# Performance work log

Measured on AMD Instinct MI355X. Metric: run time of the kernel, lower is better.

## Reference

```python
import jax, jax.numpy as jnp
import numpy as np
import math

DIM = 256
B, T = 4, 4096

def setup_inputs() -> dict:
    key = jax.random.key(0)
    ks = jax.random.split(key, 16)
    d = DIM
    def lin(k, dout, din):
        bound = 1.0 / math.sqrt(din)
        kw, kb = jax.random.split(k)
        W = jax.random.uniform(kw, (dout, din), minval=-bound, maxval=bound, dtype=jnp.float32)
        b = jax.random.uniform(kb, (dout,), minval=-bound, maxval=bound, dtype=jnp.float32)
        return W, b
    x = jax.random.normal(ks[0], (B, T, d), dtype=jnp.float32)
    wq, bq = lin(ks[1], d, d)
    wk, bk = lin(ks[2], d, d)
    wv, bv = lin(ks[3], d, d)
    wo, bo = lin(ks[4], d, d)
    w1, b1 = lin(ks[5], 4 * d, d)
    w2, b2 = lin(ks[6], d, 4 * d)
    return {
        "x": x,
        "attn_norm_w": jnp.ones((d,), jnp.float32),
        "mlp_norm_w": jnp.ones((d,), jnp.float32),
        "wq": wq, "bq": bq, "wk": wk, "bk": bk, "wv": wv, "bv": bv,
        "wo": wo, "bo": bo, "w1": w1, "b1": b1, "w2": w2, "b2": b2,
    }

def _rms_norm(x, w, eps=1e-6):
    rms = jnp.sqrt(jnp.mean(x * x, axis=-1, keepdims=True) + eps)
    return x / rms * w

def reference(x, attn_norm_w, mlp_norm_w, wq, bq, wk, bk, wv, bv, wo, bo, w1, b1, w2, b2):
    b, t, d = x.shape
    xn = _rms_norm(x, attn_norm_w)
    q = xn @ wq.T + bq  # [b,t,d]
    k = xn @ wk.T + bk
    v = xn @ wv.T + bv
    scores = jnp.einsum('btd,bsd->bts', q, k) / math.sqrt(d)
    causal = jnp.tril(jnp.ones((t, t), dtype=bool))
    scores = jnp.where(causal, scores, -1e9)
    probs = jax.nn.softmax(scores, axis=-1)
    attn = jnp.einsum('bts,bsd->btd', probs, v)
    x = x + attn @ wo.T + bo
    hn = _rms_norm(x, mlp_norm_w)
    h = jax.nn.gelu(hn @ w1.T + b1, approximate=False)
    return x + h @ w2.T + b2
```

## Files before the change

### kernel.cpp

```cpp
#include <hip/hip_runtime.h>

typedef __attribute__((ext_vector_type(8))) short bfrag;
typedef __attribute__((ext_vector_type(4))) float f32x4;

__device__ __forceinline__ f32x4 mfma16(bfrag a, bfrag b, f32x4 c) {
    return __builtin_amdgcn_mfma_f32_16x16x32_bf16(a, b, c, 0, 0, 0);
}
__device__ __forceinline__ unsigned short f2bf(float f) {
    unsigned int u = __float_as_uint(f);
    u = u + 0x7fffu + ((u >> 16) & 1u);
    return (unsigned short)(u >> 16);
}
__device__ __forceinline__ void glds16(const unsigned short* g, unsigned short* l) {
    __builtin_amdgcn_global_load_lds(
        (const __attribute__((address_space(1))) void*)g,
        (__attribute__((address_space(3))) void*)l, 16, 0, 0);
}

#define DIM 256
#define BT  16384
#define TSEQ 4096
#define FB   1048576


__global__ __launch_bounds__(256) void k_prep(
    const float* __restrict__ x, const float* __restrict__ anw,
    const float* __restrict__ wq, const float* __restrict__ wk,
    const float* __restrict__ wv, const float* __restrict__ wo,
    const float* __restrict__ w1, const float* __restrict__ w2,
    unsigned short* __restrict__ wqF, unsigned short* __restrict__ wkF,
    unsigned short* __restrict__ wvF, unsigned short* __restrict__ woF,
    unsigned short* __restrict__ w1F, unsigned short* __restrict__ w2F,
    unsigned short* __restrict__ xnF)
{
    int bid = blockIdx.x;
    int wave = threadIdx.x >> 6, lane = threadIdx.x & 63;
    int q = lane >> 4, r = lane & 15;
    if (bid < 384) {
        int fid = bid * 4 + wave;
        const float* src; unsigned short* dst; int ntile, ks, K, fbase;
        if (fid < 512) {
            int w = fid >> 7, fl = fid & 127;
            ntile = fl >> 3; ks = fl & 7; K = 256;
            src = (w == 0) ? wq : (w == 1) ? wk : (w == 2) ? wv : wo;
            dst = (w == 0) ? wqF : (w == 1) ? wkF : (w == 2) ? wvF : woF;
            fbase = (ntile * 8 + ks) * 512;
        } else if (fid < 1024) {
            int fl = fid - 512;
            ntile = fl >> 3; ks = fl & 7; K = 256;
            src = w1; dst = w1F;
            fbase = (ntile * 8 + ks) * 512;
        } else {
            int fl = fid - 1024;
            ntile = fl >> 5; ks = fl & 31; K = 1024;
            src = w2; dst = w2F;
            fbase = (ntile * 32 + ks) * 512;
        }
        const float* s = src + (ntile * 16 + r) * K + ks * 32 + q * 8;
        float4 v0 = *(const float4*)(s);
        float4 v1 = *(const float4*)(s + 4);
        unsigned short o[8] = { f2bf(v0.x), f2bf(v0.y), f2bf(v0.z), f2bf(v0.w),
                                f2bf(v1.x), f2bf(v1.y), f2bf(v1.z), f2bf(v1.w) };
        *(ushort4*)(dst + fbase + lane * 8)     = make_ushort4(o[0], o[1], o[2], o[3]);
        *(ushort4*)(dst + fbase + lane * 8 + 4) = make_ushort4(o[4], o[5], o[6], o[7]);
    } else {
        int row  = (bid - 384) * 4 + wave;
        float4 v = *(const float4*)(x + row * DIM + lane * 4);
        float ss = v.x*v.x + v.y*v.y + v.z*v.z + v.w*v.w;
        #pragma unroll
        for (int off = 1; off < 64; off <<= 1) ss += __shfl_xor(ss, off);
        float inv = rsqrtf(ss * (1.0f / DIM) + 1e-6f);
        float4 w = *(const float4*)(anw + lane * 4);
        ushort4 o = make_ushort4(f2bf(v.x*inv*w.x), f2bf(v.y*inv*w.y),
                                 f2bf(v.z*inv*w.z), f2bf(v.w*inv*w.w));
        int c = lane * 4;
        int ks = c >> 5, qp = (c >> 3) & 3, e0 = c & 7;
        *(ushort4*)(xnF + (((row >> 4) * 8 + ks) * 512) + ((qp * 16 + (row & 15)) * 8) + e0) = o;
    }
}

__global__ __launch_bounds__(256) void k_qkv(
    const unsigned short* __restrict__ xnF,
    const unsigned short* __restrict__ wqF, const unsigned short* __restrict__ wkF,
    const unsigned short* __restrict__ wvF,
    const float* __restrict__ bq, const float* __restrict__ bk, const float* __restrict__ bv,
    unsigned short* __restrict__ Q, unsigned short* __restrict__ KF,
    unsigned short* __restrict__ VF)
{
    int bid = blockIdx.x;
    int wave = threadIdx.x >> 6, lane = threadIdx.x & 63;
    int m0 = (bid / 3) * 64;
    int n0 = (bid % 3) * 256 + wave * 64;
    int wsel = n0 >> 8;
    int nc   = n0 & 255;
    const unsigned short* WF = (wsel == 0) ? wqF : (wsel == 1) ? wkF : wvF;
    const float* bias        = (wsel == 0) ? bq  : (wsel == 1) ? bk  : bv;
    int q = lane >> 4, r = lane & 15;
    int lane8 = lane * 8;
    int mt = m0 >> 4, nt = nc >> 4;

    f32x4 acc[4][4] = {};
    for (int ks = 0; ks < 8; ++ks) {
        bfrag a[4], b[4];
        #pragma unroll
        for (int i = 0; i < 4; ++i) a[i] = *(const bfrag*)(xnF + ((mt + i) * 8 + ks) * 512 + lane8);
        #pragma unroll
        for (int j = 0; j < 4; ++j) b[j] = *(const bfrag*)(WF  + ((nt + j) * 8 + ks) * 512 + lane8);
        #pragma unroll
        for (int i = 0; i < 4; ++i)
            #pragma unroll
            for (int j = 0; j < 4; ++j) acc[i][j] = mfma16(a[i], b[j], acc[i][j]);
    }

    if (wsel == 0) {
        #pragma unroll
        for (int j = 0; j < 4; ++j) {
            int col = nc + j * 16 + r;
            float bz = bias[col];
            #pragma unroll
            for (int i = 0; i < 4; ++i)
                #pragma unroll
                for (int g = 0; g < 4; ++g) {
                    int row = m0 + i * 16 + q * 4 + g;
                    Q[row * DIM + col] = f2bf(acc[i][j][g] + bz);
                }
        }
    } else if (wsel == 1) {
        #pragma unroll
        for (int j = 0; j < 4; ++j) {
            int col = nc + j * 16 + r;
            int ks = col >> 5, qc = (col >> 3) & 3, e = col & 7;
            float bz = bias[col];
            #pragma unroll
            for (int i = 0; i < 4; ++i)
                #pragma unroll
                for (int g = 0; g < 4; ++g) {
                    int row = m0 + i * 16 + q * 4 + g;
                    int bb = row >> 12;
                    int r5 = row & 31, tile = (row & 4095) >> 5;
                    int h = (r5 >> 2) & 1;
                    int rc = ((r5 >> 3) << 2) | (r5 & 3);
                    KF[bb * FB + (tile * 16 + ks * 2 + h) * 512 + (qc * 16 + rc) * 8 + e]
                        = f2bf(acc[i][j][g] + bz);
                }
        }
    } else {
        #pragma unroll
        for (int j = 0; j < 4; ++j) {
            int vd = nc + j * 16 + r;
            int jc = vd >> 4, rc = vd & 15;
            float bz = bias[vd];
            #pragma unroll
            for (int i = 0; i < 4; ++i) {
                int t0 = m0 + i * 16 + q * 4;
                int bb = t0 >> 12, tl = t0 & (TSEQ - 1);
                int tile = tl >> 5, qc = (tl >> 3) & 3, e0 = tl & 7;
                ushort4 o = make_ushort4(f2bf(acc[i][j][0] + bz), f2bf(acc[i][j][1] + bz),
                                         f2bf(acc[i][j][2] + bz), f2bf(acc[i][j][3] + bz));
                *(ushort4*)(VF + bb * FB + (tile * 16 + jc) * 512 + (qc * 16 + rc) * 8 + e0) = o;
            }
        }
    }
}

__global__ __launch_bounds__(128, 1) void k_attn(
    const unsigned short* __restrict__ Q, const unsigned short* __restrict__ KF,
    const unsigned short* __restrict__ VF, unsigned short* __restrict__ AOF)
{
    __shared__ __align__(16) unsigned char arena[65536];
    int bid = blockIdx.x;
    int xcd = bid & 7;
    int batch = xcd >> 1;
    int qt = 255 - (((bid >> 3) << 1) | (xcd & 1));
    int wave = threadIdx.x >> 6;
    int lane = threadIdx.x & 63;
    int q = lane >> 4, r = lane & 15;
    int q0 = qt * 16;
    const unsigned short* Qb  = Q  + (size_t)batch * TSEQ * DIM;
    const unsigned short* KFb = KF + (size_t)batch * FB;
    const unsigned short* VFb = VF + (size_t)batch * FB;
    int lane8 = lane * 8;

    unsigned short* Kl = (unsigned short*)(arena + wave * 32768);
    unsigned short* Vl = Kl + 8192;

    bfrag qf[8];
    #pragma unroll
    for (int ks = 0; ks < 8; ++ks)
        qf[ks] = *(const bfrag*)(Qb + (q0 + r) * DIM + ks * 32 + q * 8);

    f32x4 o[16] = {};
    float lsum = 0.f;

    int ktiles = (q0 + 16 + 31) >> 5;
    int half = ktiles >> 1, rem = ktiles & 1;
    int cnt   = half + (wave == 0 ? rem : 0);
    int start = (wave == 0) ? 0 : half + rem;

    if (cnt > 0) {
        const unsigned short* kg = KFb + (size_t)start * 8192;
        #pragma unroll
        for (int f = 0; f < 16; ++f) glds16(kg + f * 512 + lane8, Kl + f * 512);
        const unsigned short* vg = VFb + (size_t)start * 8192;
        #pragma unroll
        for (int j = 0; j < 16; ++j) glds16(vg + j * 512 + lane8, Vl + j * 512);
    }

    for (int i = 0; i < cnt; ++i) {
        int kt = start + i;
        bool more = (i + 1 < cnt);
        asm volatile("s_waitcnt vmcnt(16)" ::: "memory");
        bfrag kb0[8], kb1[8];
        #pragma unroll
        for (int ks = 0; ks < 8; ++ks) {
            kb0[ks] = *(const bfrag*)(Kl + (ks * 2    ) * 512 + lane8);
            kb1[ks] = *(const bfrag*)(Kl + (ks * 2 + 1) * 512 + lane8);
        }
        f32x4 s0 = {}, s1 = {};
        #pragma unroll
        for (int ks = 0; ks < 8; ++ks) {
            s0 = mfma16(kb0[ks], qf[ks], s0);
            s1 = mfma16(kb1[ks], qf[ks], s1);
        }
        if (more) {
            asm volatile("s_waitcnt lgkmcnt(0)" ::: "memory");
            const unsigned short* kg = KFb + (size_t)(kt + 1) * 8192;
            #pragma unroll
            for (int f = 0; f < 16; ++f) glds16(kg + f * 512 + lane8, Kl + f * 512);
        }
        int kk0 = kt * 32;
        bool lastt = (kt == ktiles - 1);
        int qglob = q0 + r;
        bfrag pf;
        #pragma unroll
        for (int g = 0; g < 4; ++g) {
            int key0 = kk0 + q * 8 + g;
            float p0 = (lastt && key0     > qglob) ? 0.f : __expf(s0[g] * 0.0625f);
            float p1 = (lastt && key0 + 4 > qglob) ? 0.f : __expf(s1[g] * 0.0625f);
            lsum += p0 + p1;
            pf[g]     = (short)f2bf(p0);
            pf[g + 4] = (short)f2bf(p1);
        }
        if (more) asm volatile("s_waitcnt vmcnt(16)" ::: "memory");
        else      asm volatile("s_waitcnt vmcnt(0)"  ::: "memory");
        #pragma unroll
        for (int j = 0; j < 16; ++j) {
            bfrag vb = *(const bfrag*)(Vl + j * 512 + lane8);
            o[j] = mfma16(pf, vb, o[j]);
        }
        if (more) {
            asm volatile("s_waitcnt lgkmcnt(0)" ::: "memory");
            const unsigned short* vg = VFb + (size_t)(kt + 1) * 8192;
            #pragma unroll
            for (int j = 0; j < 16; ++j) glds16(vg + j * 512 + lane8, Vl + j * 512);
        }
    }

    lsum += __shfl_xor(lsum, 16);
    lsum += __shfl_xor(lsum, 32);
    __syncthreads();
    float* Obuf = (float*)arena;
    float* Lbuf = (float*)(arena + 16 * 260 * 4);
    if (wave == 0) {
        if (lane < 16) Lbuf[lane] = lsum;
        #pragma unroll
        for (int j = 0; j < 16; ++j)
            #pragma unroll
            for (int g = 0; g < 4; ++g)
                Obuf[(q * 4 + g) * 260 + j * 16 + r] = o[j][g];
    }
    __syncthreads();
    if (wave == 1) {
        if (lane < 16) Lbuf[lane] += lsum;
        #pragma unroll
        for (int j = 0; j < 16; ++j)
            #pragma unroll
            for (int g = 0; g < 4; ++g)
                Obuf[(q * 4 + g) * 260 + j * 16 + r] += o[j][g];
    }
    __syncthreads();

    float linv[4];
    #pragma unroll
    for (int g = 0; g < 4; ++g) linv[g] = 1.0f / Lbuf[q * 4 + g];
    unsigned short* AOt = AOF + (size_t)(batch * 256 + qt) * 8 * 512;
    #pragma unroll
    for (int jj = 0; jj < 8; ++jj) {
        int j = wave * 8 + jj;
        int d = j * 16 + r;
        int ks = d >> 5, qp = (d >> 3) & 3, e = d & 7;
        #pragma unroll
        for (int g = 0; g < 4; ++g)
            AOt[ks * 512 + (qp * 16 + q * 4 + g) * 8 + e] =
                f2bf(Obuf[(q * 4 + g) * 260 + j * 16 + r] * linv[g]);
    }
}

__global__ __launch_bounds__(256) void k_wo(
    const unsigned short* __restrict__ AOF, const unsigned short* __restrict__ woF,
    const float* __restrict__ bo, const float* __restrict__ x,
    const float* __restrict__ mnw, float* __restrict__ x2,
    unsigned short* __restrict__ hnF)
{
    int bid = blockIdx.x;
    int wave = threadIdx.x >> 6, lane = threadIdx.x & 63;
    int m0 = bid * 64 + wave * 16;
    int mt = bid * 4 + wave;
    int q = lane >> 4, r = lane & 15;
    int lane8 = lane * 8;
    f32x4 acc[16] = {};
    for (int ks = 0; ks < 8; ++ks) {
        bfrag a = *(const bfrag*)(AOF + (mt * 8 + ks) * 512 + lane8);
        #pragma unroll
        for (int j = 0; j < 16; ++j) {
            bfrag b = *(const bfrag*)(woF + (j * 8 + ks) * 512 + lane8);
            acc[j] = mfma16(a, b, acc[j]);
        }
    }
    float ss[4] = {0.f, 0.f, 0.f, 0.f};
    #pragma unroll
    for (int j = 0; j < 16; ++j) {
        int n = j * 16 + r;
        float bz = bo[n];
        #pragma unroll
        for (int g = 0; g < 4; ++g) {
            int row = m0 + q * 4 + g;
            float v = acc[j][g] + bz + x[row * DIM + n];
            acc[j][g] = v;
            ss[g] += v * v;
            x2[row * DIM + n] = v;
        }
    }
    #pragma unroll
    for (int g = 0; g < 4; ++g) {
        #pragma unroll
        for (int off = 1; off < 16; off <<= 1) ss[g] += __shfl_xor(ss[g], off);
    }
    #pragma unroll
    for (int j = 0; j < 16; ++j) {
        int n = j * 16 + r;
        int ks = n >> 5, qp = (n >> 3) & 3, e = n & 7;
        float wn = mnw[n];
        #pragma unroll
        for (int g = 0; g < 4; ++g) {
            float inv = rsqrtf(ss[g] * (1.0f / DIM) + 1e-6f);
            hnF[(mt * 8 + ks) * 512 + (qp * 16 + q * 4 + g) * 8 + e]
                = f2bf(acc[j][g] * inv * wn);
        }
    }
}

__global__ __launch_bounds__(256) void k_w1(
    const unsigned short* __restrict__ hnF, const unsigned short* __restrict__ w1F,
    const float* __restrict__ b1, unsigned short* __restrict__ hF)
{
    int bid = blockIdx.x;
    int wave = threadIdx.x >> 6, lane = threadIdx.x & 63;
    int m0 = (bid >> 2) * 64;
    int n0 = (bid & 3) * 256 + wave * 64;
    int mt = m0 >> 4, nt = n0 >> 4;
    int q = lane >> 4, r = lane & 15;
    int lane8 = lane * 8;
    f32x4 acc[4][4] = {};
    for (int ks = 0; ks < 8; ++ks) {
        bfrag a[4], b[4];
        #pragma unroll
        for (int i = 0; i < 4; ++i) a[i] = *(const bfrag*)(hnF + ((mt + i) * 8 + ks) * 512 + lane8);
        #pragma unroll
        for (int j = 0; j < 4; ++j) b[j] = *(const bfrag*)(w1F + ((nt + j) * 8 + ks) * 512 + lane8);
        #pragma unroll
        for (int i = 0; i < 4; ++i)
            #pragma unroll
            for (int j = 0; j < 4; ++j) acc[i][j] = mfma16(a[i], b[j], acc[i][j]);
    }
    #pragma unroll
    for (int j = 0; j < 4; ++j) {
        int n = n0 + j * 16 + r;
        int ks = n >> 5, qp = (n >> 3) & 3, e = n & 7;
        float bz = b1[n];
        #pragma unroll
        for (int i = 0; i < 4; ++i)
            #pragma unroll
            for (int g = 0; g < 4; ++g) {
                float v = acc[i][j][g] + bz;
                float ge = 0.5f * v * (1.0f + erff(v * 0.70710678118654752f));
                hF[((mt + i) * 32 + ks) * 512 + (qp * 16 + q * 4 + g) * 8 + e] = f2bf(ge);
            }
    }
}

__global__ __launch_bounds__(256) void k_w2(
    const unsigned short* __restrict__ hF, const unsigned short* __restrict__ w2F,
    const float* __restrict__ b2, const float* __restrict__ x2,
    float* __restrict__ out)
{
    int bid = blockIdx.x;
    int wave = threadIdx.x >> 6, lane = threadIdx.x & 63;
    int m0 = bid * 64;
    int n0 = wave * 64;
    int mt = m0 >> 4, nt = n0 >> 4;
    int q = lane >> 4, r = lane & 15;
    int lane8 = lane * 8;
    f32x4 acc[4][4] = {};
    for (int ks = 0; ks < 32; ++ks) {
        bfrag a[4], b[4];
        #pragma unroll
        for (int i = 0; i < 4; ++i) a[i] = *(const bfrag*)(hF  + ((mt + i) * 32 + ks) * 512 + lane8);
        #pragma unroll
        for (int j = 0; j < 4; ++j) b[j] = *(const bfrag*)(w2F + ((nt + j) * 32 + ks) * 512 + lane8);
        #pragma unroll
        for (int i = 0; i < 4; ++i)
            #pragma unroll
            for (int j = 0; j < 4; ++j) acc[i][j] = mfma16(a[i], b[j], acc[i][j]);
    }
    #pragma unroll
    for (int j = 0; j < 4; ++j) {
        int n = n0 + j * 16 + r;
        float bz = b2[n];
        #pragma unroll
        for (int i = 0; i < 4; ++i)
            #pragma unroll
            for (int g = 0; g < 4; ++g) {
                int row = m0 + i * 16 + q * 4 + g;
                out[row * DIM + n] = acc[i][j][g] + bz + x2[row * DIM + n];
            }
    }
}

#define OFF_WQB 0u
#define OFF_WKB 131072u
#define OFF_WVB 262144u
#define OFF_WOB 393216u
#define OFF_W1B 524288u
#define OFF_W2B 1048576u
#define OFF_XN  1572864u
#define OFF_Q   9961472u
#define OFF_KF  18350080u
#define OFF_VF  26738688u
#define OFF_AO  35127296u
#define OFF_X2  43515904u
#define OFF_HN  60293120u
#define OFF_H   OFF_XN

extern "C" void kernel_launch(void* const* d_in, const int* in_sizes, int n_in,
                              void* d_out, int out_size, void* d_ws, size_t ws_size,
                              hipStream_t stream) {
    const float* x   = (const float*)d_in[0];
    const float* anw = (const float*)d_in[1];
    const float* mnw = (const float*)d_in[2];
    const float* wq  = (const float*)d_in[3];
    const float* bq  = (const float*)d_in[4];
    const float* wk  = (const float*)d_in[5];
    const float* bk  = (const float*)d_in[6];
    const float* wv  = (const float*)d_in[7];
    const float* bv  = (const float*)d_in[8];
    const float* wo  = (const float*)d_in[9];
    const float* bo  = (const float*)d_in[10];
    const float* w1  = (const float*)d_in[11];
    const float* b1  = (const float*)d_in[12];
    const float* w2  = (const float*)d_in[13];
    const float* b2  = (const float*)d_in[14];
    float* out = (float*)d_out;

    char* ws = (char*)d_ws;
    unsigned short* wqF = (unsigned short*)(ws + OFF_WQB);
    unsigned short* wkF = (unsigned short*)(ws + OFF_WKB);
    unsigned short* wvF = (unsigned short*)(ws + OFF_WVB);
    unsigned short* woF = (unsigned short*)(ws + OFF_WOB);
    unsigned short* w1F = (unsigned short*)(ws + OFF_W1B);
    unsigned short* w2F = (unsigned short*)(ws + OFF_W2B);
    unsigned short* xnF = (unsigned short*)(ws + OFF_XN);
    unsigned short* Qp  = (unsigned short*)(ws + OFF_Q);
    unsigned short* KFp = (unsigned short*)(ws + OFF_KF);
    unsigned short* VFp = (unsigned short*)(ws + OFF_VF);
    unsigned short* AOF = (unsigned short*)(ws + OFF_AO);
    float*          x2  = (float*)         (ws + OFF_X2);
    unsigned short* hnF = (unsigned short*)(ws + OFF_HN);
    unsigned short* hFp = (unsigned short*)(ws + OFF_H);

    k_prep<<<dim3(4480), dim3(256), 0, stream>>>(x, anw, wq, wk, wv, wo, w1, w2,
                                                 wqF, wkF, wvF, woF, w1F, w2F, xnF);
    k_qkv <<<dim3(768),  dim3(256), 0, stream>>>(xnF, wqF, wkF, wvF, bq, bk, bv, Qp, KFp, VFp);
    k_attn<<<dim3(1024), dim3(128), 0, stream>>>(Qp, KFp, VFp, AOF);
    k_wo  <<<dim3(256),  dim3(256), 0, stream>>>(AOF, woF, bo, x, mnw, x2, hnF);
    k_w1  <<<dim3(1024), dim3(256), 0, stream>>>(hnF, w1F, b1, hFp);
    k_w2  <<<dim3(256),  dim3(256), 0, stream>>>(hFp, w2F, b2, x2, out);
}
```

Before: 276.7 us.

## Double-buffer GEMM operand tiles in LDS via global_load_lds in four projection kernels

The QKV, Wo, W1 and W2 GEMM kernels now stage each K-step's A and B fragment tiles into a double-buffered shared-memory array with direct global-to-LDS loads. The next step is prefetched while MFMAs run on the current buffer, synchronised with vmcnt waits and barriers. Each wave previously fetched its own copy of the A fragments from global memory, so this shares them across the block and overlaps load latency with compute. In exchange it adds two barriers per K-step and LDS occupancy pressure, and it relies on the hand-written vmcnt counts being exact.

```diff
diff --git a/kernel.cpp b/kernel.cpp
--- a/kernel.cpp
+++ b/kernel.cpp
@@ -79,6 +79,7 @@
     }
 }
 
+
 __global__ __launch_bounds__(256) void k_qkv(
     const unsigned short* __restrict__ xnF,
     const unsigned short* __restrict__ wqF, const unsigned short* __restrict__ wkF,
@@ -87,32 +88,51 @@
     unsigned short* __restrict__ Q, unsigned short* __restrict__ KF,
     unsigned short* __restrict__ VF)
 {
+    __shared__ __align__(16) unsigned short sb[2][20 * 512];
     int bid = blockIdx.x;
     int wave = threadIdx.x >> 6, lane = threadIdx.x & 63;
     int m0 = (bid / 3) * 64;
-    int n0 = (bid % 3) * 256 + wave * 64;
-    int wsel = n0 >> 8;
-    int nc   = n0 & 255;
-    const unsigned short* WF = (wsel == 0) ? wqF : (wsel == 1) ? wkF : wvF;
-    const float* bias        = (wsel == 0) ? bq  : (wsel == 1) ? bk  : bv;
+    int grp = bid % 3;
+    int nc  = wave * 64;
+    const unsigned short* WF = (grp == 0) ? wqF : (grp == 1) ? wkF : wvF;
+    const float* bias        = (grp == 0) ? bq  : (grp == 1) ? bk  : bv;
     int q = lane >> 4, r = lane & 15;
     int lane8 = lane * 8;
-    int mt = m0 >> 4, nt = nc >> 4;
+    int mt = m0 >> 4;
+
+    #define QKV_STAGE(ks, buf)                                                   \
+        { int _k = (ks);                                                         \
+          _Pragma("unroll")                                                      \
+          for (int t = 0; t < 5; ++t) {                                          \
+              int f = wave * 5 + t;                                              \
+              const unsigned short* g = (f < 4)                                  \
+                  ? xnF + ((mt + f) * 8 + _k) * 512                              \
+                  : WF  + ((f - 4) * 8 + _k) * 512;                              \
+              glds16(g + lane8, &sb[buf][f * 512]);                              \
+          } }
 
     f32x4 acc[4][4] = {};
+    QKV_STAGE(0, 0)
     for (int ks = 0; ks < 8; ++ks) {
+        int cur = ks & 1;
+        if (ks + 1 < 8) { QKV_STAGE(ks + 1, cur ^ 1) }
+        if (ks + 1 < 8) asm volatile("s_waitcnt vmcnt(5)" ::: "memory");
+        else            asm volatile("s_waitcnt vmcnt(0)" ::: "memory");
+        asm volatile("s_barrier" ::: "memory");
         bfrag a[4], b[4];
         #pragma unroll
-        for (int i = 0; i < 4; ++i) a[i] = *(const bfrag*)(xnF + ((mt + i) * 8 + ks) * 512 + lane8);
-        #pragma unroll
-        for (int j = 0; j < 4; ++j) b[j] = *(const bfrag*)(WF  + ((nt + j) * 8 + ks) * 512 + lane8);
+        for (int i = 0; i < 4; ++i) a[i] = *(const bfrag*)(&sb[cur][i * 512] + lane8);
+        #pragma unroll
+        for (int j = 0; j < 4; ++j) b[j] = *(const bfrag*)(&sb[cur][(4 + wave * 4 + j) * 512] + lane8);
         #pragma unroll
         for (int i = 0; i < 4; ++i)
             #pragma unroll
             for (int j = 0; j < 4; ++j) acc[i][j] = mfma16(a[i], b[j], acc[i][j]);
-    }
-
-    if (wsel == 0) {
+        asm volatile("s_barrier" ::: "memory");
+    }
+    #undef QKV_STAGE
+
+    if (grp == 0) {
         #pragma unroll
         for (int j = 0; j < 4; ++j) {
             int col = nc + j * 16 + r;
@@ -125,7 +145,7 @@
                     Q[row * DIM + col] = f2bf(acc[i][j][g] + bz);
                 }
         }
-    } else if (wsel == 1) {
+    } else if (grp == 1) {
         #pragma unroll
         for (int j = 0; j < 4; ++j) {
             int col = nc + j * 16 + r;
@@ -302,21 +322,44 @@
     const float* __restrict__ mnw, float* __restrict__ x2,
     unsigned short* __restrict__ hnF)
 {
+    __shared__ __align__(16) unsigned short sb[2][20 * 512];
     int bid = blockIdx.x;
     int wave = threadIdx.x >> 6, lane = threadIdx.x & 63;
     int m0 = bid * 64 + wave * 16;
     int mt = bid * 4 + wave;
+    int mtB = bid * 4;
     int q = lane >> 4, r = lane & 15;
     int lane8 = lane * 8;
+
+    #define WO_STAGE(ks, buf)                                                    \
+        { int _k = (ks);                                                         \
+          _Pragma("unroll")                                                      \
+          for (int t = 0; t < 5; ++t) {                                          \
+              int f = wave * 5 + t;                                              \
+              const unsigned short* g = (f < 4)                                  \
+                  ? AOF + ((mtB + f) * 8 + _k) * 512                             \
+                  : woF + ((f - 4) * 8 + _k) * 512;                              \
+              glds16(g + lane8, &sb[buf][f * 512]);                              \
+          } }
+
     f32x4 acc[16] = {};
+    WO_STAGE(0, 0)
     for (int ks = 0; ks < 8; ++ks) {
-        bfrag a = *(const bfrag*)(AOF + (mt * 8 + ks) * 512 + lane8);
+        int cur = ks & 1;
+        if (ks + 1 < 8) { WO_STAGE(ks + 1, cur ^ 1) }
+        if (ks + 1 < 8) asm volatile("s_waitcnt vmcnt(5)" ::: "memory");
+        else            asm volatile("s_waitcnt vmcnt(0)" ::: "memory");
+        asm volatile("s_barrier" ::: "memory");
+        bfrag a = *(const bfrag*)(&sb[cur][wave * 512] + lane8);
         #pragma unroll
         for (int j = 0; j < 16; ++j) {
-            bfrag b = *(const bfrag*)(woF + (j * 8 + ks) * 512 + lane8);
+            bfrag b = *(const bfrag*)(&sb[cur][(4 + j) * 512] + lane8);
             acc[j] = mfma16(a, b, acc[j]);
         }
-    }
+        asm volatile("s_barrier" ::: "memory");
+    }
+    #undef WO_STAGE
+
     float ss[4] = {0.f, 0.f, 0.f, 0.f};
     #pragma unroll
     for (int j = 0; j < 16; ++j) {
@@ -354,25 +397,47 @@
     const unsigned short* __restrict__ hnF, const unsigned short* __restrict__ w1F,
     const float* __restrict__ b1, unsigned short* __restrict__ hF)
 {
+    __shared__ __align__(16) unsigned short sb[2][20 * 512];
     int bid = blockIdx.x;
     int wave = threadIdx.x >> 6, lane = threadIdx.x & 63;
     int m0 = (bid >> 2) * 64;
     int n0 = (bid & 3) * 256 + wave * 64;
-    int mt = m0 >> 4, nt = n0 >> 4;
+    int mt = m0 >> 4, ntb = (bid & 3) * 16;
     int q = lane >> 4, r = lane & 15;
     int lane8 = lane * 8;
+
+    #define W1_STAGE(ks, buf)                                                    \
+        { int _k = (ks);                                                         \
+          _Pragma("unroll")                                                      \
+          for (int t = 0; t < 5; ++t) {                                          \
+              int f = wave * 5 + t;                                              \
+              const unsigned short* g = (f < 4)                                  \
+                  ? hnF + ((mt + f) * 8 + _k) * 512                              \
+                  : w1F + ((ntb + f - 4) * 8 + _k) * 512;                        \
+              glds16(g + lane8, &sb[buf][f * 512]);                              \
+          } }
+
     f32x4 acc[4][4] = {};
+    W1_STAGE(0, 0)
     for (int ks = 0; ks < 8; ++ks) {
+        int cur = ks & 1;
+        if (ks + 1 < 8) { W1_STAGE(ks + 1, cur ^ 1) }
+        if (ks + 1 < 8) asm volatile("s_waitcnt vmcnt(5)" ::: "memory");
+        else            asm volatile("s_waitcnt vmcnt(0)" ::: "memory");
+        asm volatile("s_barrier" ::: "memory");
         bfrag a[4], b[4];
         #pragma unroll
-        for (int i = 0; i < 4; ++i) a[i] = *(const bfrag*)(hnF + ((mt + i) * 8 + ks) * 512 + lane8);
-        #pragma unroll
-        for (int j = 0; j < 4; ++j) b[j] = *(const bfrag*)(w1F + ((nt + j) * 8 + ks) * 512 + lane8);
+        for (int i = 0; i < 4; ++i) a[i] = *(const bfrag*)(&sb[cur][i * 512] + lane8);
+        #pragma unroll
+        for (int j = 0; j < 4; ++j) b[j] = *(const bfrag*)(&sb[cur][(4 + wave * 4 + j) * 512] + lane8);
         #pragma unroll
         for (int i = 0; i < 4; ++i)
             #pragma unroll
             for (int j = 0; j < 4; ++j) acc[i][j] = mfma16(a[i], b[j], acc[i][j]);
-    }
+        asm volatile("s_barrier" ::: "memory");
+    }
+    #undef W1_STAGE
+
     #pragma unroll
     for (int j = 0; j < 4; ++j) {
         int n = n0 + j * 16 + r;
@@ -394,25 +459,47 @@
     const float* __restrict__ b2, const float* __restrict__ x2,
     float* __restrict__ out)
 {
+    __shared__ __align__(16) unsigned short sb[2][20 * 512];
     int bid = blockIdx.x;
     int wave = threadIdx.x >> 6, lane = threadIdx.x & 63;
     int m0 = bid * 64;
     int n0 = wave * 64;
-    int mt = m0 >> 4, nt = n0 >> 4;
+    int mt = m0 >> 4;
     int q = lane >> 4, r = lane & 15;
     int lane8 = lane * 8;
+
+    #define W2_STAGE(ks, buf)                                                    \
+        { int _k = (ks);                                                         \
+          _Pragma("unroll")                                                      \
+          for (int t = 0; t < 5; ++t) {                                          \
+              int f = wave * 5 + t;                                              \
+              const unsigned short* g = (f < 4)                                  \
+                  ? hF  + ((mt + f) * 32 + _k) * 512                             \
+                  : w2F + ((f - 4) * 32 + _k) * 512;                             \
+              glds16(g + lane8, &sb[buf][f * 512]);                              \
+          } }
+
     f32x4 acc[4][4] = {};
+    W2_STAGE(0, 0)
     for (int ks = 0; ks < 32; ++ks) {
+        int cur = ks & 1;
+        if (ks + 1 < 32) { W2_STAGE(ks + 1, cur ^ 1) }
+        if (ks + 1 < 32) asm volatile("s_waitcnt vmcnt(5)" ::: "memory");
+        else             asm volatile("s_waitcnt vmcnt(0)" ::: "memory");
+        asm volatile("s_barrier" ::: "memory");
         bfrag a[4], b[4];
         #pragma unroll
-        for (int i = 0; i < 4; ++i) a[i] = *(const bfrag*)(hF  + ((mt + i) * 32 + ks) * 512 + lane8);
-        #pragma unroll
-        for (int j = 0; j < 4; ++j) b[j] = *(const bfrag*)(w2F + ((nt + j) * 32 + ks) * 512 + lane8);
+        for (int i = 0; i < 4; ++i) a[i] = *(const bfrag*)(&sb[cur][i * 512] + lane8);
+        #pragma unroll
+        for (int j = 0; j < 4; ++j) b[j] = *(const bfrag*)(&sb[cur][(4 + wave * 4 + j) * 512] + lane8);
         #pragma unroll
         for (int i = 0; i < 4; ++i)
             #pragma unroll
             for (int j = 0; j < 4; ++j) acc[i][j] = mfma16(a[i], b[j], acc[i][j]);
-    }
+        asm volatile("s_barrier" ::: "memory");
+    }
+    #undef W2_STAGE
+
     #pragma unroll
     for (int j = 0; j < 4; ++j) {
         int n = n0 + j * 16 + r;
```

Measured after the change: 281.4 us. No clear change (+1.7%).
